# Performance work log

Hardware: AMD Instinct MI355X
Metric: run time of the kernel (lower is better)

The kernel has to match this reference:

```python
import jax, jax.numpy as jnp
import numpy as np

INPDIM = 512
RECDIM = 512


def setup_inputs() -> dict:
    key = jax.random.key(0)
    k1, k2, k3, k4 = jax.random.split(key, 4)
    x = jax.random.normal(k1, (64, 1024, INPDIM), dtype=jnp.float32)
    W = jax.random.normal(k2, (INPDIM, RECDIM), dtype=jnp.float32) / np.sqrt(INPDIM)
    # per-unit recurrent weight vector, kept in (-1, 1) for stability
    u = jax.random.uniform(k3, (RECDIM,), dtype=jnp.float32, minval=-1.0, maxval=1.0)
    b = jax.random.normal(k4, (RECDIM,), dtype=jnp.float32) * 0.01
    return {"x": x, "W": W, "u": u, "b": b}


def reference(x, W, u, b):
    # IndRNN: h_t = relu(x_t @ W + u * h_{t-1} + b), h_0 = ones(recdim)
    B, T, _ = x.shape
    # Batch the input projection as one big GEMM (time-independent part).
    xp = jnp.einsum('bti,ir->btr', x, W) + b  # [B, T, R]
    h0 = jnp.ones((B, W.shape[1]), dtype=x.dtype)

    def step(h, xp_t):
        h = jax.nn.relu(xp_t + u * h)
        return h, h

    _, hs = jax.lax.scan(step, h0, jnp.swapaxes(xp, 0, 1))  # hs: [T, B, R]
    return jnp.swapaxes(hs, 0, 1)  # [B, T, R]
```

## Files before the change

### kernel.cpp

```cpp
#include <hip/hip_runtime.h>
#include <hip/hip_fp16.h>
#include <stdint.h>

#define TILE 128
#define BK 32
#define LDST 40

typedef __attribute__((ext_vector_type(8))) short short8;
typedef __attribute__((ext_vector_type(8))) unsigned short ushort8;
typedef __attribute__((ext_vector_type(4))) float f32x4;

static __device__ __forceinline__ unsigned short f2bf(float f) {
    union { float f; uint32_t u; } v; v.f = f;
    uint32_t u = v.u;
    u += 0x7fffu + ((u >> 16) & 1u);
    return (unsigned short)(u >> 16);
}

__global__ __launch_bounds__(256)
void wt_kernel(const float* __restrict__ W, unsigned short* __restrict__ Wt)
{
    __shared__ float s[32][33];
    const int tx = threadIdx.x;
    const int ty = threadIdx.y;
    const int kBase = blockIdx.x * 32;
    const int nBase = blockIdx.y * 32;
    #pragma unroll
    for (int j = 0; j < 4; ++j)
        s[ty + 8 * j][tx] = W[(size_t)(kBase + ty + 8 * j) * 512 + nBase + tx];
    __syncthreads();
    #pragma unroll
    for (int j = 0; j < 4; ++j)
        Wt[(size_t)(nBase + ty + 8 * j) * 512 + kBase + tx] = f2bf(s[tx][ty + 8 * j]);
}

template <bool F16OUT>
__global__ __launch_bounds__(256, 2)
void gemm_bias_kernel(const float* __restrict__ X, const unsigned short* __restrict__ Wt,
                      const float* __restrict__ bias,
                      float* __restrict__ out32, __half* __restrict__ out16)
{
    __shared__ unsigned short As[TILE * LDST];
    __shared__ unsigned short Bs[TILE * LDST];

    const int tid = threadIdx.x;
    const int colBase = blockIdx.x * TILE;
    const int rowBase = blockIdx.y * TILE;

    const int wave  = tid >> 6;
    const int lane  = tid & 63;
    const int m16   = lane & 15;
    const int quad  = lane >> 4;
    const int waveM = wave & 1;
    const int waveN = wave >> 1;

    f32x4 acc[4][4] = {};

    const int srow = tid >> 2;
    const int sc4  = tid & 3;

    for (int kt = 0; kt < 512; kt += BK) {
        #pragma unroll
        for (int p = 0; p < 2; ++p) {
            int r = p * 64 + srow;
            const float* src = X + (size_t)(rowBase + r) * 512 + kt + sc4 * 8;
            float4 v0 = *(const float4*)(src);
            float4 v1 = *(const float4*)(src + 4);
            ushort8 us;
            us[0] = f2bf(v0.x); us[1] = f2bf(v0.y); us[2] = f2bf(v0.z); us[3] = f2bf(v0.w);
            us[4] = f2bf(v1.x); us[5] = f2bf(v1.y); us[6] = f2bf(v1.z); us[7] = f2bf(v1.w);
            *(ushort8*)(&As[r * LDST + sc4 * 8]) = us;
        }
        #pragma unroll
        for (int p = 0; p < 2; ++p) {
            int n = p * 64 + srow;
            ushort8 v = *(const ushort8*)(Wt + (size_t)(colBase + n) * 512 + kt + sc4 * 8);
            *(ushort8*)(&Bs[n * LDST + sc4 * 8]) = v;
        }
        __syncthreads();

        short8 a_frag[4], b_frag[4];
        #pragma unroll
        for (int mi = 0; mi < 4; ++mi)
            a_frag[mi] = *(const short8*)&As[(waveM * 64 + mi * 16 + m16) * LDST + quad * 8];
        #pragma unroll
        for (int ni = 0; ni < 4; ++ni)
            b_frag[ni] = *(const short8*)&Bs[(waveN * 64 + ni * 16 + m16) * LDST + quad * 8];

        #pragma unroll
        for (int mi = 0; mi < 4; ++mi)
            #pragma unroll
            for (int ni = 0; ni < 4; ++ni)
                acc[mi][ni] = __builtin_amdgcn_mfma_f32_16x16x32_bf16(
                    a_frag[mi], b_frag[ni], acc[mi][ni], 0, 0, 0);
        __syncthreads();
    }

    #pragma unroll
    for (int ni = 0; ni < 4; ++ni) {
        int col = colBase + waveN * 64 + ni * 16 + m16;
        float bv = bias[col];
        #pragma unroll
        for (int mi = 0; mi < 4; ++mi) {
            int row0 = rowBase + waveM * 64 + mi * 16 + quad * 4;
            #pragma unroll
            for (int r = 0; r < 4; ++r) {
                float v = acc[mi][ni][r] + bv;
                if (F16OUT) out16[(size_t)(row0 + r) * 512 + col] = __float2half_rn(v);
                else        out32[(size_t)(row0 + r) * 512 + col] = v;
            }
        }
    }
}

#define UNR 32

__global__ __launch_bounds__(64)
void scan_f16_kernel(const __half* __restrict__ xp, float* __restrict__ out,
                     const float* __restrict__ u)
{
    const int gid = blockIdx.x * 64 + threadIdx.x;
    const int b = gid >> 9;
    const int r = gid & 511;
    const float ur = u[r];
    const unsigned short* p16 = (const unsigned short*)xp + (size_t)b * 1024 * 512 + r;
    float* po = out + (size_t)b * 1024 * 512 + r;

    float h = 1.0f;
    unsigned short cur[UNR], nxt[UNR];
    #pragma unroll
    for (int j = 0; j < UNR; ++j) cur[j] = p16[(size_t)j * 512];

    for (int t0 = 0; t0 < 1024; t0 += UNR) {
        const bool more = (t0 + UNR) < 1024;
        const unsigned short* pn = p16 + (size_t)(t0 + UNR) * 512;
        if (more) {
            #pragma unroll
            for (int j = 0; j < UNR; ++j) nxt[j] = pn[(size_t)j * 512];
        }
        #pragma unroll
        for (int j = 0; j < UNR; ++j) {
            float xv = __half2float(__ushort_as_half(cur[j]));
            h = fmaxf(fmaf(ur, h, xv), 0.0f);
            po[(size_t)(t0 + j) * 512] = h;
        }
        #pragma unroll
        for (int j = 0; j < UNR; ++j) cur[j] = nxt[j];
    }
}

__global__ __launch_bounds__(64)
void scan_f32_kernel(float* __restrict__ out, const float* __restrict__ u)
{
    const int gid = blockIdx.x * 64 + threadIdx.x;
    const int b = gid >> 9;
    const int r = gid & 511;
    const float ur = u[r];
    float* p = out + (size_t)b * 1024 * 512 + r;

    float h = 1.0f;
    float cur[UNR], nxt[UNR];
    #pragma unroll
    for (int j = 0; j < UNR; ++j) cur[j] = p[(size_t)j * 512];

    for (int t0 = 0; t0 < 1024; t0 += UNR) {
        const bool more = (t0 + UNR) < 1024;
        const float* pn = p + (size_t)(t0 + UNR) * 512;
        if (more) {
            #pragma unroll
            for (int j = 0; j < UNR; ++j) nxt[j] = pn[(size_t)j * 512];
        }
        #pragma unroll
        for (int j = 0; j < UNR; ++j) {
            h = fmaxf(fmaf(ur, h, cur[j]), 0.0f);
            p[(size_t)(t0 + j) * 512] = h;
        }
        #pragma unroll
        for (int j = 0; j < UNR; ++j) cur[j] = nxt[j];
    }
}

extern "C" void kernel_launch(void* const* d_in, const int* in_sizes, int n_in,
                              void* d_out, int out_size, void* d_ws, size_t ws_size,
                              hipStream_t stream) {
    const float* x = (const float*)d_in[0];
    const float* W = (const float*)d_in[1];
    const float* u = (const float*)d_in[2];
    const float* b = (const float*)d_in[3];
    float* out = (float*)d_out;

    const size_t WT_BYTES = (size_t)512 * 512 * 2;
    const size_t XP_BYTES = (size_t)64 * 1024 * 512 * 2;
    unsigned short* Wt = (unsigned short*)d_ws;
    __half* xp16 = (__half*)((char*)d_ws + WT_BYTES);
    const bool f16path = ws_size >= WT_BYTES + XP_BYTES;

    dim3 tgrid(16, 16), tblk(32, 8);
    wt_kernel<<<tgrid, tblk, 0, stream>>>(W, Wt);

    dim3 grid(512 / TILE, 65536 / TILE);
    if (f16path) {
        gemm_bias_kernel<true><<<grid, 256, 0, stream>>>(x, Wt, b, nullptr, xp16);
        scan_f16_kernel<<<512, 64, 0, stream>>>(xp16, out, u);
    } else {
        gemm_bias_kernel<false><<<grid, 256, 0, stream>>>(x, Wt, b, out, nullptr);
        scan_f32_kernel<<<512, 64, 0, stream>>>(out, u);
    }
}
```

Measured before the change: 330.6 us.

## Store GEMM output time-major per unit and vectorize scan loads with nontemporal stores

The GEMM now writes the fp16 projection transposed to [B, R, T], so each scan thread reads contiguous 16-byte vectors along time instead of strided 2-byte loads. The scan unroll grows to 128 steps and its fp32 output uses nontemporal stores. The GEMM grid is flattened and remapped so consecutive rows land on the same XCD, and the launch bound asks for 4 blocks per SM. The trade-offs are uncoalesced 8-byte scattered stores in the GEMM epilogue and higher register pressure in both kernels.

```diff
diff --git a/kernel.cpp b/kernel.cpp
--- a/kernel.cpp
+++ b/kernel.cpp
@@ -35,17 +35,21 @@
 }
 
 template <bool F16OUT>
-__global__ __launch_bounds__(256, 2)
+__global__ __launch_bounds__(256, 4)
 void gemm_bias_kernel(const float* __restrict__ X, const unsigned short* __restrict__ Wt,
                       const float* __restrict__ bias,
-                      float* __restrict__ out32, __half* __restrict__ out16)
+                      float* __restrict__ out32, __half* __restrict__ xpT)
 {
     __shared__ unsigned short As[TILE * LDST];
     __shared__ unsigned short Bs[TILE * LDST];
 
     const int tid = threadIdx.x;
-    const int colBase = blockIdx.x * TILE;
-    const int rowBase = blockIdx.y * TILE;
+
+    const int lin = blockIdx.x;
+    const int xcd = lin & 7;
+    const int idx = lin >> 3;
+    const int rowBase = (xcd * 64 + (idx >> 2)) * TILE;
+    const int colBase = (idx & 3) * TILE;
 
     const int wave  = tid >> 6;
     const int lane  = tid & 63;
@@ -103,52 +107,65 @@
         #pragma unroll
         for (int mi = 0; mi < 4; ++mi) {
             int row0 = rowBase + waveM * 64 + mi * 16 + quad * 4;
-            #pragma unroll
-            for (int r = 0; r < 4; ++r) {
-                float v = acc[mi][ni][r] + bv;
-                if (F16OUT) out16[(size_t)(row0 + r) * 512 + col] = __float2half_rn(v);
-                else        out32[(size_t)(row0 + r) * 512 + col] = v;
+            if (F16OUT) {
+                int bb = row0 >> 10;
+                int tt = row0 & 1023;
+                union { __half h[4]; uint2 u; } pk;
+                #pragma unroll
+                for (int r = 0; r < 4; ++r)
+                    pk.h[r] = __float2half_rn(acc[mi][ni][r] + bv);
+                *(uint2*)(xpT + ((size_t)bb * 512 + col) * 1024 + tt) = pk.u;
+            } else {
+                #pragma unroll
+                for (int r = 0; r < 4; ++r) {
+                    float v = acc[mi][ni][r] + bv;
+                    out32[(size_t)(row0 + r) * 512 + col] = v;
+                }
             }
         }
     }
 }
 
-#define UNR 32
+#define SUNR 128
 
 __global__ __launch_bounds__(64)
-void scan_f16_kernel(const __half* __restrict__ xp, float* __restrict__ out,
-                     const float* __restrict__ u)
+void scan_t_kernel(const __half* __restrict__ xpT, float* __restrict__ out,
+                   const float* __restrict__ u)
 {
     const int gid = blockIdx.x * 64 + threadIdx.x;
     const int b = gid >> 9;
     const int r = gid & 511;
     const float ur = u[r];
-    const unsigned short* p16 = (const unsigned short*)xp + (size_t)b * 1024 * 512 + r;
+    const unsigned short* p = (const unsigned short*)xpT + ((size_t)b * 512 + r) * 1024;
     float* po = out + (size_t)b * 1024 * 512 + r;
 
     float h = 1.0f;
-    unsigned short cur[UNR], nxt[UNR];
-    #pragma unroll
-    for (int j = 0; j < UNR; ++j) cur[j] = p16[(size_t)j * 512];
-
-    for (int t0 = 0; t0 < 1024; t0 += UNR) {
-        const bool more = (t0 + UNR) < 1024;
-        const unsigned short* pn = p16 + (size_t)(t0 + UNR) * 512;
+    ushort8 cur[SUNR / 8], nxt[SUNR / 8];
+    #pragma unroll
+    for (int j = 0; j < SUNR / 8; ++j) cur[j] = *(const ushort8*)(p + j * 8);
+
+    for (int t0 = 0; t0 < 1024; t0 += SUNR) {
+        const bool more = (t0 + SUNR) < 1024;
         if (more) {
             #pragma unroll
-            for (int j = 0; j < UNR; ++j) nxt[j] = pn[(size_t)j * 512];
-        }
-        #pragma unroll
-        for (int j = 0; j < UNR; ++j) {
-            float xv = __half2float(__ushort_as_half(cur[j]));
-            h = fmaxf(fmaf(ur, h, xv), 0.0f);
-            po[(size_t)(t0 + j) * 512] = h;
-        }
-        #pragma unroll
-        for (int j = 0; j < UNR; ++j) cur[j] = nxt[j];
-    }
-}
-
+            for (int j = 0; j < SUNR / 8; ++j)
+                nxt[j] = *(const ushort8*)(p + t0 + SUNR + j * 8);
+        }
+        #pragma unroll
+        for (int j = 0; j < SUNR / 8; ++j) {
+            #pragma unroll
+            for (int e = 0; e < 8; ++e) {
+                float xv = __half2float(__ushort_as_half(cur[j][e]));
+                h = fmaxf(fmaf(ur, h, xv), 0.0f);
+                __builtin_nontemporal_store(h, po + (size_t)(t0 + j * 8 + e) * 512);
+            }
+        }
+        #pragma unroll
+        for (int j = 0; j < SUNR / 8; ++j) cur[j] = nxt[j];
+    }
+}
+
+#define UNR 32
 __global__ __launch_bounds__(64)
 void scan_f32_kernel(float* __restrict__ out, const float* __restrict__ u)
 {
@@ -198,10 +215,10 @@
     dim3 tgrid(16, 16), tblk(32, 8);
     wt_kernel<<<tgrid, tblk, 0, stream>>>(W, Wt);
 
-    dim3 grid(512 / TILE, 65536 / TILE);
+    dim3 grid(2048);
     if (f16path) {
         gemm_bias_kernel<true><<<grid, 256, 0, stream>>>(x, Wt, b, nullptr, xp16);
-        scan_f16_kernel<<<512, 64, 0, stream>>>(xp16, out, u);
+        scan_t_kernel<<<512, 64, 0, stream>>>(xp16, out, u);
     } else {
         gemm_bias_kernel<false><<<grid, 256, 0, stream>>>(x, Wt, b, out, nullptr);
         scan_f32_kernel<<<512, 64, 0, stream>>>(out, u);
```

Result: faster. 308.3 us (-6.8%).

## Fuse input-projection GEMM with recurrent scan in one kernel per batch/column slice

Applied to the files above, without the earlier changes.

Replaces the separate GEMM and scan kernels with one fused kernel. Each block owns one batch and a 64-column slice, computes the projection for 128 timesteps at a time into shared memory, then one wave runs the recurrence and writes output with nontemporal stores. This removes the round trip of the intermediate projection through global memory and one kernel launch, and the block index is remapped so blocks group by XCD. The cost is that X is reread once per column slice (8 times), and only one wave of 256 threads does the serial scan while the others sit idle.

```diff
diff --git a/kernel.cpp b/kernel.cpp
--- a/kernel.cpp
+++ b/kernel.cpp
@@ -2,9 +2,10 @@
 #include <hip/hip_fp16.h>
 #include <stdint.h>
 
-#define TILE 128
-#define BK 32
-#define LDST 40
+#define BKF 64
+#define ALD 72
+#define BLD 72
+#define XLD 68
 
 typedef __attribute__((ext_vector_type(8))) short short8;
 typedef __attribute__((ext_vector_type(8))) unsigned short ushort8;
@@ -34,18 +35,23 @@
         Wt[(size_t)(nBase + ty + 8 * j) * 512 + kBase + tx] = f2bf(s[tx][ty + 8 * j]);
 }
 
-template <bool F16OUT>
 __global__ __launch_bounds__(256, 2)
-void gemm_bias_kernel(const float* __restrict__ X, const unsigned short* __restrict__ Wt,
-                      const float* __restrict__ bias,
-                      float* __restrict__ out32, __half* __restrict__ out16)
+void fused_kernel(const float* __restrict__ X, const unsigned short* __restrict__ Wt,
+                  const float* __restrict__ bias, const float* __restrict__ u,
+                  float* __restrict__ out)
 {
-    __shared__ unsigned short As[TILE * LDST];
-    __shared__ unsigned short Bs[TILE * LDST];
+    __shared__ unsigned short As[128 * ALD];
+    __shared__ unsigned short Bs[64 * BLD];
+    __shared__ float Xp[128 * XLD];
 
     const int tid = threadIdx.x;
-    const int colBase = blockIdx.x * TILE;
-    const int rowBase = blockIdx.y * TILE;
+
+    const int lin = blockIdx.x;
+    const int xcd = lin & 7;
+    const int idx = lin >> 3;
+    const int bb  = xcd * 8 + (idx >> 3);
+    const int rg  = idx & 7;
+    const int rBase = rg * 64;
 
     const int wave  = tid >> 6;
     const int lane  = tid & 63;
@@ -54,129 +60,91 @@
     const int waveM = wave & 1;
     const int waveN = wave >> 1;
 
-    f32x4 acc[4][4] = {};
+    const int sar = tid >> 1;
+    const int sak = (tid & 1) * 32;
+    const int sbr = tid >> 2;
+    const int sbk = (tid & 3) * 16;
 
-    const int srow = tid >> 2;
-    const int sc4  = tid & 3;
+    const float ur = u[rBase + lane];
+    float h = 1.0f;
+    float* po = out + ((size_t)bb * 1024) * 512 + rBase + lane;
 
-    for (int kt = 0; kt < 512; kt += BK) {
+    const float* xrow = X + ((size_t)bb * 1024 + sar) * 512 + sak;
+
+    for (int tc = 0; tc < 8; ++tc) {
+        f32x4 acc[4][2] = {};
+
+        for (int kt = 0; kt < 512; kt += BKF) {
+            {
+                const float* src = xrow + (size_t)tc * 128 * 512 + kt;
+                #pragma unroll
+                for (int q = 0; q < 4; ++q) {
+                    float4 v0 = *(const float4*)(src + q * 8);
+                    float4 v1 = *(const float4*)(src + q * 8 + 4);
+                    ushort8 us;
+                    us[0] = f2bf(v0.x); us[1] = f2bf(v0.y); us[2] = f2bf(v0.z); us[3] = f2bf(v0.w);
+                    us[4] = f2bf(v1.x); us[5] = f2bf(v1.y); us[6] = f2bf(v1.z); us[7] = f2bf(v1.w);
+                    *(ushort8*)(&As[sar * ALD + sak + q * 8]) = us;
+                }
+            }
+            {
+                const unsigned short* src = Wt + (size_t)(rBase + sbr) * 512 + kt + sbk;
+                *(ushort8*)(&Bs[sbr * BLD + sbk])     = *(const ushort8*)(src);
+                *(ushort8*)(&Bs[sbr * BLD + sbk + 8]) = *(const ushort8*)(src + 8);
+            }
+            __syncthreads();
+
+            short8 xf[4][2], wf[2][2];
+            #pragma unroll
+            for (int mi = 0; mi < 4; ++mi)
+                #pragma unroll
+                for (int kh = 0; kh < 2; ++kh)
+                    xf[mi][kh] = *(const short8*)&As[(waveM * 64 + mi * 16 + m16) * ALD + kh * 32 + quad * 8];
+            #pragma unroll
+            for (int ni = 0; ni < 2; ++ni)
+                #pragma unroll
+                for (int kh = 0; kh < 2; ++kh)
+                    wf[ni][kh] = *(const short8*)&Bs[(waveN * 32 + ni * 16 + m16) * BLD + kh * 32 + quad * 8];
+
+            #pragma unroll
+            for (int mi = 0; mi < 4; ++mi)
+                #pragma unroll
+                for (int ni = 0; ni < 2; ++ni)
+                    #pragma unroll
+                    for (int kh = 0; kh < 2; ++kh)
+                        acc[mi][ni] = __builtin_amdgcn_mfma_f32_16x16x32_bf16(
+                            wf[ni][kh], xf[mi][kh], acc[mi][ni], 0, 0, 0);
+            __syncthreads();
+        }
+
         #pragma unroll
-        for (int p = 0; p < 2; ++p) {
-            int r = p * 64 + srow;
-            const float* src = X + (size_t)(rowBase + r) * 512 + kt + sc4 * 8;
-            float4 v0 = *(const float4*)(src);
-            float4 v1 = *(const float4*)(src + 4);
-            ushort8 us;
-            us[0] = f2bf(v0.x); us[1] = f2bf(v0.y); us[2] = f2bf(v0.z); us[3] = f2bf(v0.w);
-            us[4] = f2bf(v1.x); us[5] = f2bf(v1.y); us[6] = f2bf(v1.z); us[7] = f2bf(v1.w);
-            *(ushort8*)(&As[r * LDST + sc4 * 8]) = us;
-        }
-        #pragma unroll
-        for (int p = 0; p < 2; ++p) {
-            int n = p * 64 + srow;
-            ushort8 v = *(const ushort8*)(Wt + (size_t)(colBase + n) * 512 + kt + sc4 * 8);
-            *(ushort8*)(&Bs[n * LDST + sc4 * 8]) = v;
+        for (int ni = 0; ni < 2; ++ni) {
+            int r0 = waveN * 32 + ni * 16 + quad * 4;
+            float4 b4 = *(const float4*)&bias[rBase + r0];
+            #pragma unroll
+            for (int mi = 0; mi < 4; ++mi) {
+                int t = waveM * 64 + mi * 16 + m16;
+                f32x4 v = acc[mi][ni];
+                v[0] += b4.x; v[1] += b4.y; v[2] += b4.z; v[3] += b4.w;
+                *(f32x4*)&Xp[t * XLD + r0] = v;
+            }
         }
         __syncthreads();
 
-        short8 a_frag[4], b_frag[4];
-        #pragma unroll
-        for (int mi = 0; mi < 4; ++mi)
-            a_frag[mi] = *(const short8*)&As[(waveM * 64 + mi * 16 + m16) * LDST + quad * 8];
-        #pragma unroll
-        for (int ni = 0; ni < 4; ++ni)
-            b_frag[ni] = *(const short8*)&Bs[(waveN * 64 + ni * 16 + m16) * LDST + quad * 8];
-
-        #pragma unroll
-        for (int mi = 0; mi < 4; ++mi)
-            #pragma unroll
-            for (int ni = 0; ni < 4; ++ni)
-                acc[mi][ni] = __builtin_amdgcn_mfma_f32_16x16x32_bf16(
-                    a_frag[mi], b_frag[ni], acc[mi][ni], 0, 0, 0);
-        __syncthreads();
-    }
-
-    #pragma unroll
-    for (int ni = 0; ni < 4; ++ni) {
-        int col = colBase + waveN * 64 + ni * 16 + m16;
-        float bv = bias[col];
-        #pragma unroll
-        for (int mi = 0; mi < 4; ++mi) {
-            int row0 = rowBase + waveM * 64 + mi * 16 + quad * 4;
-            #pragma unroll
-            for (int r = 0; r < 4; ++r) {
-                float v = acc[mi][ni][r] + bv;
-                if (F16OUT) out16[(size_t)(row0 + r) * 512 + col] = __float2half_rn(v);
-                else        out32[(size_t)(row0 + r) * 512 + col] = v;
+        if (tid < 64) {
+            float* pt = po + (size_t)tc * 128 * 512;
+            #pragma unroll 1
+            for (int t8 = 0; t8 < 128; t8 += 16) {
+                float v[16];
+                #pragma unroll
+                for (int i = 0; i < 16; ++i) v[i] = Xp[(t8 + i) * XLD + lane];
+                #pragma unroll
+                for (int i = 0; i < 16; ++i) {
+                    h = fmaxf(fmaf(ur, h, v[i]), 0.0f);
+                    __builtin_nontemporal_store(h, pt + (size_t)(t8 + i) * 512);
+                }
             }
         }
-    }
-}
-
-#define UNR 32
-
-__global__ __launch_bounds__(64)
-void scan_f16_kernel(const __half* __restrict__ xp, float* __restrict__ out,
-                     const float* __restrict__ u)
-{
-    const int gid = blockIdx.x * 64 + threadIdx.x;
-    const int b = gid >> 9;
-    const int r = gid & 511;
-    const float ur = u[r];
-    const unsigned short* p16 = (const unsigned short*)xp + (size_t)b * 1024 * 512 + r;
-    float* po = out + (size_t)b * 1024 * 512 + r;
-
-    float h = 1.0f;
-    unsigned short cur[UNR], nxt[UNR];
-    #pragma unroll
-    for (int j = 0; j < UNR; ++j) cur[j] = p16[(size_t)j * 512];
-
-    for (int t0 = 0; t0 < 1024; t0 += UNR) {
-        const bool more = (t0 + UNR) < 1024;
-        const unsigned short* pn = p16 + (size_t)(t0 + UNR) * 512;
-        if (more) {
-            #pragma unroll
-            for (int j = 0; j < UNR; ++j) nxt[j] = pn[(size_t)j * 512];
-        }
-        #pragma unroll
-        for (int j = 0; j < UNR; ++j) {
-            float xv = __half2float(__ushort_as_half(cur[j]));
-            h = fmaxf(fmaf(ur, h, xv), 0.0f);
-            po[(size_t)(t0 + j) * 512] = h;
-        }
-        #pragma unroll
-        for (int j = 0; j < UNR; ++j) cur[j] = nxt[j];
-    }
-}
-
-__global__ __launch_bounds__(64)
-void scan_f32_kernel(float* __restrict__ out, const float* __restrict__ u)
-{
-    const int gid = blockIdx.x * 64 + threadIdx.x;
-    const int b = gid >> 9;
-    const int r = gid & 511;
-    const float ur = u[r];
-    float* p = out + (size_t)b * 1024 * 512 + r;
-
-    float h = 1.0f;
-    float cur[UNR], nxt[UNR];
-    #pragma unroll
-    for (int j = 0; j < UNR; ++j) cur[j] = p[(size_t)j * 512];
-
-    for (int t0 = 0; t0 < 1024; t0 += UNR) {
-        const bool more = (t0 + UNR) < 1024;
-        const float* pn = p + (size_t)(t0 + UNR) * 512;
-        if (more) {
-            #pragma unroll
-            for (int j = 0; j < UNR; ++j) nxt[j] = pn[(size_t)j * 512];
-        }
-        #pragma unroll
-        for (int j = 0; j < UNR; ++j) {
-            h = fmaxf(fmaf(ur, h, cur[j]), 0.0f);
-            p[(size_t)(t0 + j) * 512] = h;
-        }
-        #pragma unroll
-        for (int j = 0; j < UNR; ++j) cur[j] = nxt[j];
     }
 }
 
@@ -189,21 +157,10 @@
     const float* b = (const float*)d_in[3];
     float* out = (float*)d_out;
 
-    const size_t WT_BYTES = (size_t)512 * 512 * 2;
-    const size_t XP_BYTES = (size_t)64 * 1024 * 512 * 2;
     unsigned short* Wt = (unsigned short*)d_ws;
-    __half* xp16 = (__half*)((char*)d_ws + WT_BYTES);
-    const bool f16path = ws_size >= WT_BYTES + XP_BYTES;
 
     dim3 tgrid(16, 16), tblk(32, 8);
     wt_kernel<<<tgrid, tblk, 0, stream>>>(W, Wt);
 
-    dim3 grid(512 / TILE, 65536 / TILE);
-    if (f16path) {
-        gemm_bias_kernel<true><<<grid, 256, 0, stream>>>(x, Wt, b, nullptr, xp16);
-        scan_f16_kernel<<<512, 64, 0, stream>>>(xp16, out, u);
-    } else {
-        gemm_bias_kernel<false><<<grid, 256, 0, stream>>>(x, Wt, b, out, nullptr);
-        scan_f32_kernel<<<512, 64, 0, stream>>>(out, u);
-    }
+    fused_kernel<<<512, 256, 0, stream>>>(x, Wt, b, u, out);
 }
```

New measurement: 384.2 us. +16.2%, slower.
